# Performance work log

Hardware: AMD Instinct MI355X
Metric: run time of the kernel (lower is better)

The kernel has to match this reference:

```python
import jax, jax.numpy as jnp
import numpy as np

B, T, C = 8, 1024, 768
NH = 12
HD = C // NH  # 64


def setup_inputs() -> dict:
    key = jax.random.key(0)
    k1, k2, k3 = jax.random.split(key, 3)
    x = jax.random.normal(k1, (B, T, C), dtype=jnp.float32)
    w_attn = jax.random.normal(k2, (C, 3 * C), dtype=jnp.float32) * 0.02
    b_attn = jnp.zeros((3 * C,), dtype=jnp.float32)
    w_proj = jax.random.normal(k3, (C, C), dtype=jnp.float32) * 0.02
    b_proj = jnp.zeros((C,), dtype=jnp.float32)
    return {"x": x, "w_attn": w_attn, "b_attn": b_attn, "w_proj": w_proj, "b_proj": b_proj}


def reference(x, w_attn, b_attn, w_proj, b_proj):
    Bb, Tt, Cc = x.shape
    qkv = x @ w_attn + b_attn  # [B,T,3C]
    q, k, v = jnp.split(qkv, [Cc, 2 * Cc], axis=-1)
    # [B, NH, T, HD]
    q = q.reshape(Bb, Tt, NH, HD).swapaxes(1, 2)
    k = k.reshape(Bb, Tt, NH, HD).swapaxes(1, 2)
    v = v.reshape(Bb, Tt, NH, HD).swapaxes(1, 2)
    scale = 1.0 / jnp.sqrt(jnp.asarray(HD, dtype=x.dtype))
    att = jnp.einsum("bhqd,bhkd->bhqk", q, k) * scale  # [B,NH,T,T]
    causal = jnp.tril(jnp.ones((Tt, Tt), dtype=bool))[None, None]
    att = jnp.where(causal, att, jnp.asarray(-jnp.inf, dtype=att.dtype))
    att = jax.nn.softmax(att, axis=-1)
    y = jnp.einsum("bhqk,bhkd->bhqd", att, v)  # [B,NH,T,HD]
    y = y.swapaxes(1, 2).reshape(Bb, Tt, Cc)
    return y @ w_proj + b_proj
```

## Files before the change

kernel.cpp:

```cpp
#include <hip/hip_runtime.h>
#include <cstdint>
#include <cstddef>

typedef __attribute__((ext_vector_type(8))) short short8;
typedef __attribute__((ext_vector_type(4))) float f32x4;
typedef __attribute__((ext_vector_type(4))) unsigned short u16x4;

#define ASYNC16(gp, lp) \
  __builtin_amdgcn_global_load_lds((const __attribute__((address_space(1))) unsigned int*)(gp), \
                                   (__attribute__((address_space(3))) unsigned int*)(lp), 16, 0, 0)

__device__ __forceinline__ unsigned short f2b(float f) {
  union { float f; unsigned int u; } c; c.f = f;
  unsigned int u = c.u;
  return (unsigned short)((u + 0x7fffu + ((u >> 16) & 1u)) >> 16);
}


__global__ __launch_bounds__(256) void prep(
    const float* __restrict__ x, unsigned short* __restrict__ xb,
    const float* __restrict__ w_attn, unsigned short* __restrict__ waT,
    const float* __restrict__ w_proj, unsigned short* __restrict__ wpT) {
  __shared__ unsigned short Ts[64][65];
  const int bb = blockIdx.x;
  const int tid = threadIdx.x;
  if (bb < 3072) {
    int i = (bb * 256 + tid) * 8;
    const float* px = x + i;
    short8 v;
    for (int e = 0; e < 8; ++e) ((unsigned short*)&v)[e] = f2b(px[e]);
    *(short8*)(xb + i) = v;
    return;
  }
  const float* W; unsigned short* WT; int Kd, Nd, n0, k0;
  if (bb < 3504) {
    int t = bb - 3072; W = w_attn; WT = waT; Kd = 768; Nd = 2304;
    n0 = (t % 36) * 64; k0 = (t / 36) * 64;
  } else {
    int t = bb - 3504; W = w_proj; WT = wpT; Kd = 768; Nd = 768;
    n0 = (t % 12) * 64; k0 = (t / 12) * 64;
  }
  for (int idx = tid; idx < 4096; idx += 256) {
    int lr = idx >> 6, lc = idx & 63;
    Ts[lr][lc] = f2b(W[(size_t)(k0 + lr) * Nd + n0 + lc]);
  }
  __syncthreads();
  for (int idx = tid; idx < 4096; idx += 256) {
    int nr = idx >> 6, kc = idx & 63;
    WT[(size_t)(n0 + nr) * Kd + k0 + kc] = Ts[kc][nr];
  }
}


__global__ __launch_bounds__(256, 2) void gemm_qkv(
    const unsigned short* __restrict__ A,
    const unsigned short* __restrict__ Bt,
    const float* __restrict__ bias,
    unsigned short* __restrict__ q,
    unsigned short* __restrict__ k,
    unsigned short* __restrict__ vT)
{
  __shared__ unsigned short As[2][128 * 64];
  __shared__ unsigned short Bs[2][128 * 64];
  const int tid = threadIdx.x;
  const int w = tid >> 6, lane = tid & 63;
  const int wm = w >> 1, wn = w & 1;
  const int lr = lane & 15, lq = lane >> 4;

  const int bid = blockIdx.x;
  const int xcd = bid & 7;
  const int local = bid >> 3;
  const int ty = local >> 3;
  const int tx = xcd * 8 + (local & 7);
  const int m0 = tx * 128, n0 = ty * 128;
  const f32x4 fzero = {0.f, 0.f, 0.f, 0.f};

  f32x4 acc[4][4];
  for (int i = 0; i < 4; ++i) for (int j = 0; j < 4; ++j) acc[i][j] = fzero;

  const int trow = tid >> 3;
  const int tcol = (tid & 7) ^ (trow & 7);
  const unsigned short* Asrc = A + (size_t)(m0 + trow) * 768 + tcol * 8;
  const unsigned short* Bsrc = Bt + (size_t)(n0 + trow) * 768 + tcol * 8;
  const int dst0 = tid * 16;

#define STAGE_QKV(s, bidx) do { \
    const unsigned short* as_ = Asrc + (s) * 64; \
    const unsigned short* bs_ = Bsrc + (s) * 64; \
    ASYNC16(as_,            (char*)As[bidx] + dst0); \
    ASYNC16(as_ + 32 * 768, (char*)As[bidx] + dst0 + 4096); \
    ASYNC16(as_ + 64 * 768, (char*)As[bidx] + dst0 + 8192); \
    ASYNC16(as_ + 96 * 768, (char*)As[bidx] + dst0 + 12288); \
    ASYNC16(bs_,            (char*)Bs[bidx] + dst0); \
    ASYNC16(bs_ + 32 * 768, (char*)Bs[bidx] + dst0 + 4096); \
    ASYNC16(bs_ + 64 * 768, (char*)Bs[bidx] + dst0 + 8192); \
    ASYNC16(bs_ + 96 * 768, (char*)Bs[bidx] + dst0 + 12288); \
  } while (0)

  STAGE_QKV(0, 0);

  const int swz = (lq ^ (lr & 7)) * 16;
  const int arow = (wm * 64 + lr) * 128;
  const int brow = (wn * 64 + lr) * 128;

  for (int s = 0; s < 12; ++s) {
    __builtin_amdgcn_s_barrier();
    if (s + 1 < 12) {
      STAGE_QKV(s + 1, (s + 1) & 1);
      asm volatile("s_waitcnt vmcnt(8)" ::: "memory");
    } else {
      asm volatile("s_waitcnt vmcnt(0)" ::: "memory");
    }
    __builtin_amdgcn_s_barrier();
    __builtin_amdgcn_sched_barrier(0);
    const char* asb = (const char*)As[s & 1];
    const char* bsb = (const char*)Bs[s & 1];
    for (int ks = 0; ks < 2; ++ks) {
      const int cb = swz ^ (ks << 6);
      short8 a[4], b[4];
      for (int i = 0; i < 4; ++i)
        a[i] = *(const short8*)(asb + arow + i * 2048 + cb);
      for (int j = 0; j < 4; ++j)
        b[j] = *(const short8*)(bsb + brow + j * 2048 + cb);
      for (int i = 0; i < 4; ++i)
        for (int j = 0; j < 4; ++j)
          acc[i][j] = __builtin_amdgcn_mfma_f32_16x16x32_bf16(a[i], b[j], acc[i][j], 0, 0, 0);
    }
  }
#undef STAGE_QKV

  const int colbase = n0 + wn * 64;
  const int sec = colbase / 768;
  const float QSCALE = 0.18033688011112042f;
  for (int j = 0; j < 4; ++j) {
    int col = colbase + j * 16 + lr;
    int cc = col - sec * 768;
    int h = cc >> 6, d = cc & 63;
    float bv = bias[col];
    for (int i = 0; i < 4; ++i) {
      int row0 = m0 + wm * 64 + i * 16 + lq * 4;
      int bidx = row0 >> 10, t0 = row0 & 1023;
      int bh = bidx * 12 + h;
      if (sec == 0) {
        for (int r = 0; r < 4; ++r)
          q[((size_t)bh * 1024 + t0 + r) * 64 + d] = f2b((acc[i][j][r] + bv) * QSCALE);
      } else if (sec == 1) {
        for (int r = 0; r < 4; ++r)
          k[((size_t)bh * 1024 + t0 + r) * 64 + d] = f2b(acc[i][j][r] + bv);
      } else {
        u16x4 pv;
        pv[0] = f2b(acc[i][j][0] + bv);
        pv[1] = f2b(acc[i][j][1] + bv);
        pv[2] = f2b(acc[i][j][2] + bv);
        pv[3] = f2b(acc[i][j][3] + bv);
        *(u16x4*)(vT + ((size_t)bh * 64 + d) * 1024 + t0) = pv;
      }
    }
  }
}


__global__ __launch_bounds__(256, 3) void attn(
    const unsigned short* __restrict__ q,
    const unsigned short* __restrict__ kk,
    const unsigned short* __restrict__ vT,
    unsigned short* __restrict__ y)
{
  __shared__ unsigned short Qs[128 * 72];
  __shared__ unsigned short Ks[64 * 72];
  __shared__ unsigned short Vt[64 * 72];
  __shared__ unsigned short Ps[4 * 16 * 72];

  const int tid = threadIdx.x;
  const int w = tid >> 6, lane = tid & 63;
  const int lr = lane & 15, lq = lane >> 4;

  const int bid = blockIdx.x;
  const int xcd = bid & 7;
  const int local = bid >> 3;
  const int bh = xcd + 8 * (local >> 3);
  const int qp = local & 7;
  const int qt1 = 15 - qp;
  const int b = bh / 12, h = bh - b * 12;
  const f32x4 fzero = {0.f, 0.f, 0.f, 0.f};

  unsigned short* Pw = Ps + w * 16 * 72;
  const unsigned short* kbase = kk + (size_t)bh * 65536;
  const unsigned short* vbase = vT + (size_t)bh * 65536;

  {
    const unsigned short* qa = q + ((size_t)bh * 1024 + qp * 64) * 64;
    const unsigned short* qb = q + ((size_t)bh * 1024 + qt1 * 64) * 64;
    for (int c = tid; c < 512; c += 256) {
      int row = c >> 3, d0 = (c & 7) * 8;
      *(short8*)(Qs + row * 72 + d0)        = *(const short8*)(qa + (size_t)c * 8);
      *(short8*)(Qs + (row + 64) * 72 + d0) = *(const short8*)(qb + (size_t)c * 8);
    }
  }

  const int c0 = tid, c1 = tid + 256;
  short8 kreg[2], vreg[2];
  kreg[0] = *(const short8*)(kbase + (size_t)c0 * 8);
  kreg[1] = *(const short8*)(kbase + (size_t)c1 * 8);
  vreg[0] = *(const short8*)(vbase + (size_t)(c0 >> 3) * 1024 + (c0 & 7) * 8);
  vreg[1] = *(const short8*)(vbase + (size_t)(c1 >> 3) * 1024 + (c1 & 7) * 8);

  f32x4 o0[4], o1[4];
  float l0[4], l1[4];
  for (int jd = 0; jd < 4; ++jd) { o0[jd] = fzero; o1[jd] = fzero; }
  for (int r = 0; r < 4; ++r) { l0[r] = 0.0f; l1[r] = 0.0f; }

  const int nkt = qt1 + 1;

  for (int kt = 0; kt < nkt; ++kt) {
    __syncthreads();
    *(short8*)(Ks + (c0 >> 3) * 72 + (c0 & 7) * 8) = kreg[0];
    *(short8*)(Ks + (c1 >> 3) * 72 + (c1 & 7) * 8) = kreg[1];
    *(short8*)(Vt + (c0 >> 3) * 72 + (c0 & 7) * 8) = vreg[0];
    *(short8*)(Vt + (c1 >> 3) * 72 + (c1 & 7) * 8) = vreg[1];
    __syncthreads();
    if (kt + 1 < nkt) {
      const unsigned short* kp = kbase + (size_t)(kt + 1) * 4096;
      const unsigned short* vp = vbase + (size_t)(kt + 1) * 64;
      kreg[0] = *(const short8*)(kp + (size_t)c0 * 8);
      kreg[1] = *(const short8*)(kp + (size_t)c1 * 8);
      vreg[0] = *(const short8*)(vp + (size_t)(c0 >> 3) * 1024 + (c0 & 7) * 8);
      vreg[1] = *(const short8*)(vp + (size_t)(c1 >> 3) * 1024 + (c1 & 7) * 8);
    }

    short8 bk[2][4];
    for (int ks = 0; ks < 2; ++ks)
      for (int j = 0; j < 4; ++j)
        bk[ks][j] = *(const short8*)(Ks + (j * 16 + lr) * 72 + ks * 32 + lq * 8);

    if (kt <= qp) {
      f32x4 s[4];
      for (int j = 0; j < 4; ++j) s[j] = fzero;
      for (int ks = 0; ks < 2; ++ks) {
        short8 aq = *(const short8*)(Qs + (w * 16 + lr) * 72 + ks * 32 + lq * 8);
        for (int j = 0; j < 4; ++j)
          s[j] = __builtin_amdgcn_mfma_f32_16x16x32_bf16(aq, bk[ks][j], s[j], 0, 0, 0);
      }
      if (kt == qp) {
        int rowt = w * 16 + lq * 4;
        for (int j = 0; j < 4; ++j) {
          int colt = j * 16 + lr;
          for (int r = 0; r < 4; ++r)
            if (colt > rowt + r) s[j][r] = -1e30f;
        }
      }
      for (int r = 0; r < 4; ++r) {
        int prow = (lq * 4 + r) * 72;
        float acc = 0.0f;
        for (int j = 0; j < 4; ++j) {
          float p = __builtin_amdgcn_exp2f(s[j][r]);
          acc += p;
          union { float f; unsigned int u; } cv; cv.f = p;
          Pw[prow + j * 16 + lr] = (unsigned short)((cv.u + 0x8000u) >> 16);
        }
        l0[r] += acc;
      }
      for (int ks = 0; ks < 2; ++ks) {
        short8 ap = *(const short8*)(Pw + lr * 72 + ks * 32 + lq * 8);
        short8 bv[4];
        for (int jd = 0; jd < 4; ++jd)
          bv[jd] = *(const short8*)(Vt + (jd * 16 + lr) * 72 + ks * 32 + lq * 8);
        for (int jd = 0; jd < 4; ++jd)
          o0[jd] = __builtin_amdgcn_mfma_f32_16x16x32_bf16(ap, bv[jd], o0[jd], 0, 0, 0);
      }
    }

    {
      f32x4 s[4];
      for (int j = 0; j < 4; ++j) s[j] = fzero;
      for (int ks = 0; ks < 2; ++ks) {
        short8 aq = *(const short8*)(Qs + (64 + w * 16 + lr) * 72 + ks * 32 + lq * 8);
        for (int j = 0; j < 4; ++j)
          s[j] = __builtin_amdgcn_mfma_f32_16x16x32_bf16(aq, bk[ks][j], s[j], 0, 0, 0);
      }
      if (kt == qt1) {
        int rowt = w * 16 + lq * 4;
        for (int j = 0; j < 4; ++j) {
          int colt = j * 16 + lr;
          for (int r = 0; r < 4; ++r)
            if (colt > rowt + r) s[j][r] = -1e30f;
        }
      }
      for (int r = 0; r < 4; ++r) {
        int prow = (lq * 4 + r) * 72;
        float acc = 0.0f;
        for (int j = 0; j < 4; ++j) {
          float p = __builtin_amdgcn_exp2f(s[j][r]);
          acc += p;
          union { float f; unsigned int u; } cv; cv.f = p;
          Pw[prow + j * 16 + lr] = (unsigned short)((cv.u + 0x8000u) >> 16);
        }
        l1[r] += acc;
      }
      for (int ks = 0; ks < 2; ++ks) {
        short8 ap = *(const short8*)(Pw + lr * 72 + ks * 32 + lq * 8);
        short8 bv[4];
        for (int jd = 0; jd < 4; ++jd)
          bv[jd] = *(const short8*)(Vt + (jd * 16 + lr) * 72 + ks * 32 + lq * 8);
        for (int jd = 0; jd < 4; ++jd)
          o1[jd] = __builtin_amdgcn_mfma_f32_16x16x32_bf16(ap, bv[jd], o1[jd], 0, 0, 0);
      }
    }
  }

  for (int r = 0; r < 4; ++r) {
    float a0 = l0[r], a1 = l1[r];
    for (int off = 1; off < 16; off <<= 1) {
      a0 += __shfl_xor(a0, off, 16);
      a1 += __shfl_xor(a1, off, 16);
    }
    l0[r] = 1.0f / a0;
    l1[r] = 1.0f / a1;
  }
  int t0 = qp * 64 + w * 16 + lq * 4;
  int t1 = qt1 * 64 + w * 16 + lq * 4;
  for (int jd = 0; jd < 4; ++jd) {
    int d = jd * 16 + lr;
    for (int r = 0; r < 4; ++r) {
      y[((size_t)b * 1024 + t0 + r) * 768 + h * 64 + d] = f2b(o0[jd][r] * l0[r]);
      y[((size_t)b * 1024 + t1 + r) * 768 + h * 64 + d] = f2b(o1[jd][r] * l1[r]);
    }
  }
}


__global__ __launch_bounds__(256, 3) void gemm_proj(
    const unsigned short* __restrict__ A,
    const unsigned short* __restrict__ Bt,
    const float* __restrict__ bias,
    float* __restrict__ out)
{
  __shared__ unsigned short As[2][64 * 64];
  __shared__ unsigned short Bs[2][128 * 64];
  const int tid = threadIdx.x;
  const int w = tid >> 6, lane = tid & 63;
  const int wm = w >> 1, wn = w & 1;
  const int lr = lane & 15, lq = lane >> 4;

  const int bid = blockIdx.x;
  const int xcd = bid & 7;
  const int local = bid >> 3;
  const int ty = local >> 4;
  const int tx = xcd * 16 + (local & 15);
  const int m0 = tx * 64, n0 = ty * 128;
  const f32x4 fzero = {0.f, 0.f, 0.f, 0.f};

  f32x4 acc[2][4];
  for (int i = 0; i < 2; ++i) for (int j = 0; j < 4; ++j) acc[i][j] = fzero;

  const int trow = tid >> 3;
  const int tcol = (tid & 7) ^ (trow & 7);
  const unsigned short* Asrc = A + (size_t)(m0 + trow) * 768 + tcol * 8;
  const unsigned short* Bsrc = Bt + (size_t)(n0 + trow) * 768 + tcol * 8;
  const int dst0 = tid * 16;

#define STAGE_PROJ(s, bidx) do { \
    const unsigned short* as_ = Asrc + (s) * 64; \
    const unsigned short* bs_ = Bsrc + (s) * 64; \
    ASYNC16(as_,            (char*)As[bidx] + dst0); \
    ASYNC16(as_ + 32 * 768, (char*)As[bidx] + dst0 + 4096); \
    ASYNC16(bs_,            (char*)Bs[bidx] + dst0); \
    ASYNC16(bs_ + 32 * 768, (char*)Bs[bidx] + dst0 + 4096); \
    ASYNC16(bs_ + 64 * 768, (char*)Bs[bidx] + dst0 + 8192); \
    ASYNC16(bs_ + 96 * 768, (char*)Bs[bidx] + dst0 + 12288); \
  } while (0)

  STAGE_PROJ(0, 0);

  const int swz = (lq ^ (lr & 7)) * 16;
  const int arow = (wm * 32 + lr) * 128;
  const int brow = (wn * 64 + lr) * 128;

  for (int s = 0; s < 12; ++s) {
    __builtin_amdgcn_s_barrier();
    if (s + 1 < 12) {
      STAGE_PROJ(s + 1, (s + 1) & 1);
      asm volatile("s_waitcnt vmcnt(6)" ::: "memory");
    } else {
      asm volatile("s_waitcnt vmcnt(0)" ::: "memory");
    }
    __builtin_amdgcn_s_barrier();
    __builtin_amdgcn_sched_barrier(0);
    const char* asb = (const char*)As[s & 1];
    const char* bsb = (const char*)Bs[s & 1];
    for (int ks = 0; ks < 2; ++ks) {
      const int cb = swz ^ (ks << 6);
      short8 a[2], b[4];
      for (int i = 0; i < 2; ++i)
        a[i] = *(const short8*)(asb + arow + i * 2048 + cb);
      for (int j = 0; j < 4; ++j)
        b[j] = *(const short8*)(bsb + brow + j * 2048 + cb);
      for (int i = 0; i < 2; ++i)
        for (int j = 0; j < 4; ++j)
          acc[i][j] = __builtin_amdgcn_mfma_f32_16x16x32_bf16(a[i], b[j], acc[i][j], 0, 0, 0);
    }
  }
#undef STAGE_PROJ

  for (int j = 0; j < 4; ++j) {
    int col = n0 + wn * 64 + j * 16 + lr;
    float bv = bias[col];
    for (int i = 0; i < 2; ++i) {
      int row0 = m0 + wm * 32 + i * 16 + lq * 4;
      for (int r = 0; r < 4; ++r)
        out[(size_t)(row0 + r) * 768 + col] = acc[i][j][r] + bv;
    }
  }
}


extern "C" void kernel_launch(void* const* d_in, const int* in_sizes, int n_in,
                              void* d_out, int out_size, void* d_ws, size_t ws_size,
                              hipStream_t stream) {
  const float* x      = (const float*)d_in[0];
  const float* w_attn = (const float*)d_in[1];
  const float* b_attn = (const float*)d_in[2];
  const float* w_proj = (const float*)d_in[3];
  const float* b_proj = (const float*)d_in[4];
  float* out = (float*)d_out;

  char* p = (char*)d_ws;
  unsigned short* xb  = (unsigned short*)p; p += (size_t)8192 * 768 * 2;
  unsigned short* waT = (unsigned short*)p; p += (size_t)2304 * 768 * 2;
  unsigned short* wpT = (unsigned short*)p; p += (size_t)768 * 768 * 2;
  unsigned short* qb  = (unsigned short*)p; p += (size_t)96 * 1024 * 64 * 2;
  unsigned short* kb  = (unsigned short*)p; p += (size_t)96 * 1024 * 64 * 2;
  unsigned short* vTb = (unsigned short*)p; p += (size_t)96 * 64 * 1024 * 2;
  unsigned short* yb  = (unsigned short*)p; p += (size_t)8192 * 768 * 2;

  prep<<<3648, 256, 0, stream>>>(x, xb, w_attn, waT, w_proj, wpT);
  gemm_qkv<<<1152, 256, 0, stream>>>(xb, waT, b_attn, qb, kb, vTb);
  attn<<<768, 256, 0, stream>>>(qb, kb, vTb, yb);
  gemm_proj<<<768, 256, 0, stream>>>(yb, wpT, b_proj, out);
}
```

Measured before the change: 174.1 us.

## Restructure QKV GEMM into 256x128 tiles with 8 waves and ping-pong split-K pipeline

The QKV GEMM now uses 512-thread blocks, each computing a 256x128 output tile with 8 waves. The K=64 stage is split into two 32-wide halves, and async loads for the next stage are interleaved between MFMA clusters using fine-grained barriers and s_setprio. The aim is to hide global-to-LDS latency and raise MFMA issue density while halving the block count. In exchange there are many more barriers and a new swizzle pattern, and the stricter vmcnt accounting is fragile.

```diff
diff --git a/kernel.cpp b/kernel.cpp
--- a/kernel.cpp
+++ b/kernel.cpp
@@ -9,6 +9,8 @@
 #define ASYNC16(gp, lp) \
   __builtin_amdgcn_global_load_lds((const __attribute__((address_space(1))) unsigned int*)(gp), \
                                    (__attribute__((address_space(3))) unsigned int*)(lp), 16, 0, 0)
+
+#define BARM() asm volatile("s_barrier" ::: "memory")
 
 __device__ __forceinline__ unsigned short f2b(float f) {
   union { float f; unsigned int u; } c; c.f = f;
@@ -52,7 +54,7 @@
 }
 
 
-__global__ __launch_bounds__(256, 2) void gemm_qkv(
+__global__ __launch_bounds__(512, 2) void gemm_qkv(
     const unsigned short* __restrict__ A,
     const unsigned short* __restrict__ Bt,
     const float* __restrict__ bias,
@@ -60,8 +62,8 @@
     unsigned short* __restrict__ k,
     unsigned short* __restrict__ vT)
 {
-  __shared__ unsigned short As[2][128 * 64];
-  __shared__ unsigned short Bs[2][128 * 64];
+  __shared__ unsigned short Abuf[2][2][256 * 32];
+  __shared__ unsigned short Bbuf[2][2][128 * 32];
   const int tid = threadIdx.x;
   const int w = tid >> 6, lane = tid & 63;
   const int wm = w >> 1, wn = w & 1;
@@ -70,64 +72,125 @@
   const int bid = blockIdx.x;
   const int xcd = bid & 7;
   const int local = bid >> 3;
-  const int ty = local >> 3;
-  const int tx = xcd * 8 + (local & 7);
-  const int m0 = tx * 128, n0 = ty * 128;
+  const int mi = xcd * 4 + local / 18;
+  const int ni = local % 18;
+  const int m0 = mi * 256, n0 = ni * 128;
   const f32x4 fzero = {0.f, 0.f, 0.f, 0.f};
 
   f32x4 acc[4][4];
   for (int i = 0; i < 4; ++i) for (int j = 0; j < 4; ++j) acc[i][j] = fzero;
 
-  const int trow = tid >> 3;
-  const int tcol = (tid & 7) ^ (trow & 7);
-  const unsigned short* Asrc = A + (size_t)(m0 + trow) * 768 + tcol * 8;
-  const unsigned short* Bsrc = Bt + (size_t)(n0 + trow) * 768 + tcol * 8;
-  const int dst0 = tid * 16;
-
-#define STAGE_QKV(s, bidx) do { \
-    const unsigned short* as_ = Asrc + (s) * 64; \
-    const unsigned short* bs_ = Bsrc + (s) * 64; \
-    ASYNC16(as_,            (char*)As[bidx] + dst0); \
-    ASYNC16(as_ + 32 * 768, (char*)As[bidx] + dst0 + 4096); \
-    ASYNC16(as_ + 64 * 768, (char*)As[bidx] + dst0 + 8192); \
-    ASYNC16(as_ + 96 * 768, (char*)As[bidx] + dst0 + 12288); \
-    ASYNC16(bs_,            (char*)Bs[bidx] + dst0); \
-    ASYNC16(bs_ + 32 * 768, (char*)Bs[bidx] + dst0 + 4096); \
-    ASYNC16(bs_ + 64 * 768, (char*)Bs[bidx] + dst0 + 8192); \
-    ASYNC16(bs_ + 96 * 768, (char*)Bs[bidx] + dst0 + 12288); \
+  const int tr = tid >> 2;
+  const int gc = (tid & 3) ^ ((tid >> 3) & 3);
+  const unsigned short* AsrcQ = A + (size_t)(m0 + tr) * 768 + gc * 8;
+  const unsigned short* BsrcQ = Bt + (size_t)(n0 + tr) * 768 + gc * 8;
+  const int tid16 = tid * 16;
+
+#define S_A(t, h, buf) do { \
+    const unsigned short* s_ = AsrcQ + (t) * 64 + (h) * 32; \
+    ASYNC16(s_,             (char*)Abuf[buf][h] + tid16); \
+    ASYNC16(s_ + 128 * 768, (char*)Abuf[buf][h] + tid16 + 8192); \
   } while (0)
-
-  STAGE_QKV(0, 0);
-
-  const int swz = (lq ^ (lr & 7)) * 16;
-  const int arow = (wm * 64 + lr) * 128;
-  const int brow = (wn * 64 + lr) * 128;
-
-  for (int s = 0; s < 12; ++s) {
-    __builtin_amdgcn_s_barrier();
-    if (s + 1 < 12) {
-      STAGE_QKV(s + 1, (s + 1) & 1);
-      asm volatile("s_waitcnt vmcnt(8)" ::: "memory");
-    } else {
-      asm volatile("s_waitcnt vmcnt(0)" ::: "memory");
-    }
-    __builtin_amdgcn_s_barrier();
-    __builtin_amdgcn_sched_barrier(0);
-    const char* asb = (const char*)As[s & 1];
-    const char* bsb = (const char*)Bs[s & 1];
-    for (int ks = 0; ks < 2; ++ks) {
-      const int cb = swz ^ (ks << 6);
-      short8 a[4], b[4];
-      for (int i = 0; i < 4; ++i)
-        a[i] = *(const short8*)(asb + arow + i * 2048 + cb);
-      for (int j = 0; j < 4; ++j)
-        b[j] = *(const short8*)(bsb + brow + j * 2048 + cb);
-      for (int i = 0; i < 4; ++i)
-        for (int j = 0; j < 4; ++j)
-          acc[i][j] = __builtin_amdgcn_mfma_f32_16x16x32_bf16(a[i], b[j], acc[i][j], 0, 0, 0);
-    }
-  }
-#undef STAGE_QKV
+#define S_B(t, h, buf) do { \
+    const unsigned short* s_ = BsrcQ + (t) * 64 + (h) * 32; \
+    ASYNC16(s_, (char*)Bbuf[buf][h] + tid16); \
+  } while (0)
+
+  const int xv = (lr >> 1) & 3;
+  const int cb = (lq ^ xv) << 4;
+  const int aoff = (wm * 64 + lr) * 64 + cb;
+  const int boff = (wn * 64 + lr) * 64 + cb;
+
+  S_A(0, 0, 0); S_B(0, 0, 0); S_A(0, 1, 0); S_B(0, 1, 0);
+  asm volatile("s_waitcnt vmcnt(3)" ::: "memory");
+  BARM();
+
+  for (int t = 0; t < 12; ++t) {
+    const int c = t & 1, nb = c ^ 1;
+    const bool pf = (t < 11);
+    const char* Ac0 = (const char*)Abuf[c][0];
+    const char* Bc0 = (const char*)Bbuf[c][0];
+    const char* Ac1 = (const char*)Abuf[c][1];
+    const char* Bc1 = (const char*)Bbuf[c][1];
+    short8 a0, a1, a2, a3, b0, b1, b2, b3;
+
+    a0 = *(const short8*)(Ac0 + aoff);
+    a1 = *(const short8*)(Ac0 + aoff + 1024);
+    a2 = *(const short8*)(Ac0 + aoff + 2048);
+    a3 = *(const short8*)(Ac0 + aoff + 3072);
+    b0 = *(const short8*)(Bc0 + boff);
+    b1 = *(const short8*)(Bc0 + boff + 1024);
+    if (pf) S_A(t + 1, 0, nb);
+    BARM();
+    __builtin_amdgcn_s_setprio(1);
+    acc[0][0] = __builtin_amdgcn_mfma_f32_16x16x32_bf16(a0, b0, acc[0][0], 0, 0, 0);
+    acc[1][0] = __builtin_amdgcn_mfma_f32_16x16x32_bf16(a1, b0, acc[1][0], 0, 0, 0);
+    acc[2][0] = __builtin_amdgcn_mfma_f32_16x16x32_bf16(a2, b0, acc[2][0], 0, 0, 0);
+    acc[3][0] = __builtin_amdgcn_mfma_f32_16x16x32_bf16(a3, b0, acc[3][0], 0, 0, 0);
+    acc[0][1] = __builtin_amdgcn_mfma_f32_16x16x32_bf16(a0, b1, acc[0][1], 0, 0, 0);
+    acc[1][1] = __builtin_amdgcn_mfma_f32_16x16x32_bf16(a1, b1, acc[1][1], 0, 0, 0);
+    acc[2][1] = __builtin_amdgcn_mfma_f32_16x16x32_bf16(a2, b1, acc[2][1], 0, 0, 0);
+    acc[3][1] = __builtin_amdgcn_mfma_f32_16x16x32_bf16(a3, b1, acc[3][1], 0, 0, 0);
+    __builtin_amdgcn_s_setprio(0);
+    BARM();
+
+    b2 = *(const short8*)(Bc0 + boff + 2048);
+    b3 = *(const short8*)(Bc0 + boff + 3072);
+    if (pf) S_B(t + 1, 0, nb);
+    BARM();
+    __builtin_amdgcn_s_setprio(1);
+    acc[0][2] = __builtin_amdgcn_mfma_f32_16x16x32_bf16(a0, b2, acc[0][2], 0, 0, 0);
+    acc[1][2] = __builtin_amdgcn_mfma_f32_16x16x32_bf16(a1, b2, acc[1][2], 0, 0, 0);
+    acc[2][2] = __builtin_amdgcn_mfma_f32_16x16x32_bf16(a2, b2, acc[2][2], 0, 0, 0);
+    acc[3][2] = __builtin_amdgcn_mfma_f32_16x16x32_bf16(a3, b2, acc[3][2], 0, 0, 0);
+    acc[0][3] = __builtin_amdgcn_mfma_f32_16x16x32_bf16(a0, b3, acc[0][3], 0, 0, 0);
+    acc[1][3] = __builtin_amdgcn_mfma_f32_16x16x32_bf16(a1, b3, acc[1][3], 0, 0, 0);
+    acc[2][3] = __builtin_amdgcn_mfma_f32_16x16x32_bf16(a2, b3, acc[2][3], 0, 0, 0);
+    acc[3][3] = __builtin_amdgcn_mfma_f32_16x16x32_bf16(a3, b3, acc[3][3], 0, 0, 0);
+    __builtin_amdgcn_s_setprio(0);
+    if (pf) asm volatile("s_waitcnt vmcnt(3)" ::: "memory");
+    else    asm volatile("s_waitcnt vmcnt(0)" ::: "memory");
+    BARM();
+
+    a0 = *(const short8*)(Ac1 + aoff);
+    a1 = *(const short8*)(Ac1 + aoff + 1024);
+    a2 = *(const short8*)(Ac1 + aoff + 2048);
+    a3 = *(const short8*)(Ac1 + aoff + 3072);
+    b0 = *(const short8*)(Bc1 + boff);
+    b1 = *(const short8*)(Bc1 + boff + 1024);
+    if (pf) S_A(t + 1, 1, nb);
+    BARM();
+    __builtin_amdgcn_s_setprio(1);
+    acc[0][0] = __builtin_amdgcn_mfma_f32_16x16x32_bf16(a0, b0, acc[0][0], 0, 0, 0);
+    acc[1][0] = __builtin_amdgcn_mfma_f32_16x16x32_bf16(a1, b0, acc[1][0], 0, 0, 0);
+    acc[2][0] = __builtin_amdgcn_mfma_f32_16x16x32_bf16(a2, b0, acc[2][0], 0, 0, 0);
+    acc[3][0] = __builtin_amdgcn_mfma_f32_16x16x32_bf16(a3, b0, acc[3][0], 0, 0, 0);
+    acc[0][1] = __builtin_amdgcn_mfma_f32_16x16x32_bf16(a0, b1, acc[0][1], 0, 0, 0);
+    acc[1][1] = __builtin_amdgcn_mfma_f32_16x16x32_bf16(a1, b1, acc[1][1], 0, 0, 0);
+    acc[2][1] = __builtin_amdgcn_mfma_f32_16x16x32_bf16(a2, b1, acc[2][1], 0, 0, 0);
+    acc[3][1] = __builtin_amdgcn_mfma_f32_16x16x32_bf16(a3, b1, acc[3][1], 0, 0, 0);
+    __builtin_amdgcn_s_setprio(0);
+    BARM();
+
+    b2 = *(const short8*)(Bc1 + boff + 2048);
+    b3 = *(const short8*)(Bc1 + boff + 3072);
+    if (pf) S_B(t + 1, 1, nb);
+    BARM();
+    __builtin_amdgcn_s_setprio(1);
+    acc[0][2] = __builtin_amdgcn_mfma_f32_16x16x32_bf16(a0, b2, acc[0][2], 0, 0, 0);
+    acc[1][2] = __builtin_amdgcn_mfma_f32_16x16x32_bf16(a1, b2, acc[1][2], 0, 0, 0);
+    acc[2][2] = __builtin_amdgcn_mfma_f32_16x16x32_bf16(a2, b2, acc[2][2], 0, 0, 0);
+    acc[3][2] = __builtin_amdgcn_mfma_f32_16x16x32_bf16(a3, b2, acc[3][2], 0, 0, 0);
+    acc[0][3] = __builtin_amdgcn_mfma_f32_16x16x32_bf16(a0, b3, acc[0][3], 0, 0, 0);
+    acc[1][3] = __builtin_amdgcn_mfma_f32_16x16x32_bf16(a1, b3, acc[1][3], 0, 0, 0);
+    acc[2][3] = __builtin_amdgcn_mfma_f32_16x16x32_bf16(a2, b3, acc[2][3], 0, 0, 0);
+    acc[3][3] = __builtin_amdgcn_mfma_f32_16x16x32_bf16(a3, b3, acc[3][3], 0, 0, 0);
+    __builtin_amdgcn_s_setprio(0);
+    if (pf) asm volatile("s_waitcnt vmcnt(3)" ::: "memory");
+    BARM();
+  }
+#undef S_A
+#undef S_B
 
   const int colbase = n0 + wn * 64;
   const int sec = colbase / 768;
@@ -434,7 +497,7 @@
   unsigned short* yb  = (unsigned short*)p; p += (size_t)8192 * 768 * 2;
 
   prep<<<3648, 256, 0, stream>>>(x, xb, w_attn, waT, w_proj, wpT);
-  gemm_qkv<<<1152, 256, 0, stream>>>(xb, waT, b_attn, qb, kb, vTb);
+  gemm_qkv<<<576, 512, 0, stream>>>(xb, waT, b_attn, qb, kb, vTb);
   attn<<<768, 256, 0, stream>>>(qb, kb, vTb, yb);
   gemm_proj<<<768, 256, 0, stream>>>(yb, wpT, b_proj, out);
 }
```

After: 198.1 us. 1.14x slower.
